# Kernel tuning notes

Measured on AMD Instinct MI355X. Metric: run time of the kernel, lower is better.

The kernel has to match this reference:

```python
import jax, jax.numpy as jnp
import numpy as np

NUM_HEADS = 8
ATTN_DIM = 64

def setup_inputs() -> dict:
    key = jax.random.key(0)
    ks = jax.random.split(key, 16)
    C = ATTN_DIM
    inp = {
        "rgb_fea": jax.random.normal(ks[0], (2, C, 48, 48), jnp.float32),
        "depth_fea": jax.random.normal(ks[1], (2, 1, 24, 24), jnp.float32),
        # expend_conv: Conv2d(1 -> C, k=1), with bias (torch default)
        "w_exp": jax.random.normal(ks[2], (C, 1), jnp.float32) * 0.2,
        "b_exp": jax.random.normal(ks[3], (C,), jnp.float32) * 0.02,
        # q/k/v linears (no bias), weights stored torch-style [out, in]
        "w_rgb_q": jax.random.normal(ks[4], (C, C), jnp.float32) * (C ** -0.5),
        "w_rgb_k": jax.random.normal(ks[5], (C, C), jnp.float32) * (C ** -0.5),
        "w_rgb_v": jax.random.normal(ks[6], (C, C), jnp.float32) * (C ** -0.5),
        "w_dep_q": jax.random.normal(ks[7], (C, C), jnp.float32) * (C ** -0.5),
        "w_dep_k": jax.random.normal(ks[8], (C, C), jnp.float32) * (C ** -0.5),
        "w_dep_v": jax.random.normal(ks[9], (C, C), jnp.float32) * (C ** -0.5),
        # output projections (with bias)
        "w_rgb_proj": jax.random.normal(ks[10], (C, C), jnp.float32) * (C ** -0.5),
        "b_rgb_proj": jax.random.normal(ks[11], (C,), jnp.float32) * 0.02,
        "w_dep_proj": jax.random.normal(ks[12], (C, C), jnp.float32) * (C ** -0.5),
        "b_dep_proj": jax.random.normal(ks[13], (C,), jnp.float32) * 0.02,
        # compress_conv: Conv2d(2C -> C, k=1), with bias
        "w_comp": jax.random.normal(ks[14], (C, 2 * C), jnp.float32) * ((2 * C) ** -0.5),
        "b_comp": jax.random.normal(ks[15], (C,), jnp.float32) * 0.02,
    }
    return inp


def _heads(x, b, n, h):
    # [B, N, C] -> [B, H, N, C/H]
    c = x.shape[-1]
    return x.reshape(b, n, h, c // h).transpose(0, 2, 1, 3)


def reference(rgb_fea, depth_fea, w_exp, b_exp,
              w_rgb_q, w_rgb_k, w_rgb_v, w_dep_q, w_dep_k, w_dep_v,
              w_rgb_proj, b_rgb_proj, w_dep_proj, b_dep_proj,
              w_comp, b_comp):
    b, c, h, w = rgb_fea.shape
    H = NUM_HEADS
    scale = (c // H) ** -0.5

    # expend_conv (1x1) + ReLU + bilinear upsample (align_corners=False)
    d = jnp.einsum('bihw,oi->bohw', depth_fea, w_exp) + b_exp[None, :, None, None]
    d = jax.nn.relu(d)
    d = jax.image.resize(d, (b, c, h, w), method='bilinear')

    # (B,C,H,W) -> transpose(1,3) -> (B,W,H,C) -> (B, N=w*h, C)
    N = w * h
    rgb = rgb_fea.transpose(0, 3, 2, 1).reshape(b, N, c)
    dep = d.transpose(0, 3, 2, 1).reshape(b, N, c)

    rq = _heads(rgb @ w_rgb_q.T, b, N, H)
    rk = _heads(rgb @ w_rgb_k.T, b, N, H)
    rv = _heads(rgb @ w_rgb_v.T, b, N, H)
    dq = _heads(dep @ w_dep_q.T, b, N, H)
    dk = _heads(dep @ w_dep_k.T, b, N, H)
    dv = _heads(dep @ w_dep_v.T, b, N, H)

    # rgb queries attend to depth keys/values
    rgb_attn = jax.nn.softmax(jnp.einsum('bhnd,bhmd->bhnm', rq, dk) * scale, axis=-1)
    rgb_out = jnp.einsum('bhnm,bhmd->bhnd', rgb_attn, dv)
    rgb_out = rgb_out.transpose(0, 2, 1, 3).reshape(b, N, c) @ w_rgb_proj.T + b_rgb_proj

    # depth queries attend to rgb keys/values
    dep_attn = jax.nn.softmax(jnp.einsum('bhnd,bhmd->bhnm', dq, rk) * scale, axis=-1)
    dep_out = jnp.einsum('bhnm,bhmd->bhnd', dep_attn, rv)
    dep_out = dep_out.transpose(0, 2, 1, 3).reshape(b, N, c) @ w_dep_proj.T + b_dep_proj

    # (B,N,C) -> (B,C,N) -> (B,C,w,h)
    rgb_out = rgb_out.transpose(0, 2, 1).reshape(b, c, w, h)
    dep_out = dep_out.transpose(0, 2, 1).reshape(b, c, w, h)

    fuse = jnp.concatenate([rgb_out, dep_out], axis=1)
    fuse = jnp.einsum('bihw,oi->bohw', fuse, w_comp) + b_comp[None, :, None, None]
    return jax.nn.gelu(fuse, approximate=False)
```

## Files before the change

kernel.cpp:

```cpp
#include <hip/hip_runtime.h>
#include <math.h>

#define BATCH 2
#define C 64
#define HH 48
#define WW 48
#define NTOK 2304
#define HEADS 8
#define KVSTRIDE 12

typedef unsigned short bf16_t;
typedef __attribute__((ext_vector_type(8))) short bf16x8;
typedef __attribute__((ext_vector_type(4))) float f32x4;

__device__ __forceinline__ bf16_t f2bf(float f) {
    unsigned int u = __float_as_uint(f);
    u = (u + 0x7fffu + ((u >> 16) & 1u)) >> 16;
    return (bf16_t)u;
}
__device__ __forceinline__ unsigned pack2(float a, float b) {
    return (unsigned)f2bf(a) | ((unsigned)f2bf(b) << 16);
}
__device__ __forceinline__ float4 ld_bf4(const bf16_t* p) {
    uint2 v = *(const uint2*)p;
    float4 r;
    r.x = __uint_as_float(v.x << 16); r.y = __uint_as_float(v.x & 0xffff0000u);
    r.z = __uint_as_float(v.y << 16); r.w = __uint_as_float(v.y & 0xffff0000u);
    return r;
}

__device__ __forceinline__ void stage_x_row(
    float* xrow, const float* rgb, const float* dep,
    const float* w_exp, const float* b_exp,
    int b, int n, int strm, int c0, int cstep)
{
    int wi = n / HH, hi = n % HH;
    if (strm == 0) {
        const float* base = rgb + (size_t)b * C * NTOK + (size_t)hi * WW + wi;
        for (int c = c0; c < 64; c += cstep)
            xrow[c] = base[(size_t)c * NTOK];
    } else {
        float cy = 0.5f * hi - 0.25f, cx = 0.5f * wi - 0.25f;
        float fy0 = floorf(cy), fx0 = floorf(cx);
        float fy = cy - fy0, fx = cx - fx0;
        int y0 = max((int)fy0, 0), x0 = max((int)fx0, 0);
        int y1 = min((int)fy0 + 1, 23), x1 = min((int)fx0 + 1, 23);
        const float* dp = dep + b * 576;
        float d00 = dp[y0*24 + x0], d01 = dp[y0*24 + x1];
        float d10 = dp[y1*24 + x0], d11 = dp[y1*24 + x1];
        for (int c = c0; c < 64; c += cstep) {
            float w = w_exp[c], bb = b_exp[c];
            float r00 = fmaxf(w*d00 + bb, 0.f), r01 = fmaxf(w*d01 + bb, 0.f);
            float r10 = fmaxf(w*d10 + bb, 0.f), r11 = fmaxf(w*d11 + bb, 0.f);
            xrow[c] = (1.f-fy)*((1.f-fx)*r00 + fx*r01) + fy*((1.f-fx)*r10 + fx*r11);
        }
    }
}


__global__ __launch_bounds__(256) void prep_kernel(
    const float* __restrict__ rgb, const float* __restrict__ dep,
    const float* __restrict__ w_exp, const float* __restrict__ b_exp,
    const float* __restrict__ w_rp, const float* __restrict__ w_dp,
    const float* __restrict__ w_comp,
    const float* __restrict__ b_rp, const float* __restrict__ b_dp,
    const float* __restrict__ b_comp,
    float* __restrict__ Xt,
    float* __restrict__ W1, float* __restrict__ W2, float* __restrict__ beff)
{
    __shared__ float U[64*68];
    int bid = blockIdx.x;
    int tid = threadIdx.x;

    if (bid < 144) {
        int t = bid >> 2, z = bid & 3;
        int b = z >> 1, strm = z & 1;
        if (strm == 0) {
            const float* src = rgb + (size_t)b * C * NTOK + t * 64;
            #pragma unroll
            for (int p = 0; p < 4; ++p) {
                int idx = tid + p * 256;
                int c = idx >> 4, m4 = (idx & 15) * 4;
                *(float4*)&U[c*65 + m4] = *(const float4*)&src[(size_t)c * NTOK + m4];
            }
            __syncthreads();
            #pragma unroll
            for (int p = 0; p < 4; ++p) {
                int idx = tid + p * 256;
                int row = idx >> 4, l = idx & 15;
                int mi = t * 64 + row;
                int hi = mi / 48, wi = mi % 48;
                int n  = wi * 48 + hi;
                float4 v;
                v.x = U[(4*l + 0)*65 + row];
                v.y = U[(4*l + 1)*65 + row];
                v.z = U[(4*l + 2)*65 + row];
                v.w = U[(4*l + 3)*65 + row];
                *(float4*)&Xt[((size_t)z * NTOK + n) * 64 + 4*l] = v;
            }
        } else {
            int tok_l = tid >> 2, cq = (tid & 3) * 16;
            int n = t * 64 + tok_l;
            int wi = n / HH, hi = n % HH;
            float cy = 0.5f * hi - 0.25f, cx = 0.5f * wi - 0.25f;
            float fy0 = floorf(cy), fx0 = floorf(cx);
            float fy = cy - fy0, fx = cx - fx0;
            int y0 = max((int)fy0, 0), x0 = max((int)fx0, 0);
            int y1 = min((int)fy0 + 1, 23), x1 = min((int)fx0 + 1, 23);
            const float* dp = dep + b * 576;
            float d00 = dp[y0*24 + x0], d01 = dp[y0*24 + x1];
            float d10 = dp[y1*24 + x0], d11 = dp[y1*24 + x1];
            float* orow = &Xt[((size_t)z * NTOK + n) * 64];
            #pragma unroll
            for (int cc = 0; cc < 16; cc += 4) {
                float4 v;
                #pragma unroll
                for (int j = 0; j < 4; ++j) {
                    int c = cq + cc + j;
                    float w = w_exp[c], bb = b_exp[c];
                    float r00 = fmaxf(w*d00 + bb, 0.f), r01 = fmaxf(w*d01 + bb, 0.f);
                    float r10 = fmaxf(w*d10 + bb, 0.f), r11 = fmaxf(w*d11 + bb, 0.f);
                    ((float*)&v)[j] = (1.f-fy)*((1.f-fx)*r00 + fx*r01)
                                    + fy*((1.f-fx)*r10 + fx*r11);
                }
                *(float4*)&orow[cq + cc] = v;
            }
        }
    } else {
        int idx0 = bid - 144;
        int bx = idx0 & 3, m = idx0 >> 2;
        const float* Wp = m ? w_dp : w_rp;
        float* Wo = m ? W2 : W1;
        int sr = tid >> 4, sc4 = (tid & 15) * 4;
        #pragma unroll
        for (int rr = 0; rr < 4; ++rr) {
            int r = rr*16 + sr;
            *(float4*)&U[r*68 + sc4] = *(const float4*)&Wp[r*64 + sc4];
        }
        __syncthreads();
        int r = tid >> 4;
        int o = bx*16 + r;
        int c4 = (tid & 15) * 4;
        float a0 = 0, a1 = 0, a2 = 0, a3 = 0;
        for (int j = 0; j < 64; ++j) {
            float wc = w_comp[o*128 + m*64 + j];
            float4 wp = *(const float4*)&U[j*68 + c4];
            a0 += wc*wp.x; a1 += wc*wp.y; a2 += wc*wp.z; a3 += wc*wp.w;
        }
        Wo[o*64 + c4]     = a0;
        Wo[o*64 + c4 + 1] = a1;
        Wo[o*64 + c4 + 2] = a2;
        Wo[o*64 + c4 + 3] = a3;
        if (bx == 0 && m == 0 && tid < 64) {
            float s = b_comp[tid];
            for (int j = 0; j < 64; ++j)
                s += w_comp[tid*128 + j] * b_rp[j] + w_comp[tid*128 + 64 + j] * b_dp[j];
            beff[tid] = s;
        }
    }
}

__global__ __launch_bounds__(256) void qkv_kernel(
    const float* __restrict__ Xt,
    const float* __restrict__ w_rq, const float* __restrict__ w_rk,
    const float* __restrict__ w_rv,
    const float* __restrict__ w_dq, const float* __restrict__ w_dk,
    const float* __restrict__ w_dv,
    bf16_t* __restrict__ Qb, bf16_t* __restrict__ Kb, bf16_t* __restrict__ VT)
{
    int tile = blockIdx.x;
    int z    = blockIdx.y;
    int b = z >> 1, strm = z & 1;
    int sb = strm*2 + b;

    __shared__ float Xs[16][68];
    __shared__ float Ws[64][68];
    int tid = threadIdx.x;
    int sr = tid >> 4, sc = (tid & 15) * 4;

    float4 wreg[3][4];
    #pragma unroll
    for (int m = 0; m < 3; ++m) {
        const float* W = strm ? (m == 0 ? w_dq : m == 1 ? w_dk : w_dv)
                              : (m == 0 ? w_rq : m == 1 ? w_rk : w_rv);
        #pragma unroll
        for (int rr = 0; rr < 4; ++rr)
            wreg[m][rr] = *(const float4*)&W[(rr*16 + sr)*64 + sc];
    }
    {
        int row = tid >> 4, c4 = (tid & 15) * 4;
        *(float4*)&Xs[row][c4] =
            *(const float4*)&Xt[((size_t)z*NTOK + tile*16 + row)*64 + c4];
    }

    int ty = tid >> 4, tx = tid & 15;
    #pragma unroll
    for (int m = 0; m < 3; ++m) {
        __syncthreads();
        #pragma unroll
        for (int rr = 0; rr < 4; ++rr)
            *(float4*)&Ws[rr*16 + sr][sc] = wreg[m][rr];
        __syncthreads();

        float acc[4] = {};
        #pragma unroll
        for (int k = 0; k < 64; k += 4) {
            float4 xv = *(const float4*)&Xs[ty][k];
            #pragma unroll
            for (int j = 0; j < 4; ++j) {
                float4 wv = *(const float4*)&Ws[tx + 16*j][k];
                acc[j] += xv.x*wv.x + xv.y*wv.y + xv.z*wv.z + xv.w*wv.w;
            }
        }
        float scale = (m == 0) ? (0.35355339059327373f * 1.4426950408889634f) : 1.0f;
        int n = tile*16 + ty;
        #pragma unroll
        for (int j = 0; j < 4; ++j) {
            int o = tx + 16*j;
            int h = o >> 3, d = o & 7;
            bf16_t v = f2bf(acc[j] * scale);
            if (m == 0)      Qb[(((size_t)sb*8 + h)*NTOK + n)*8 + d] = v;
            else if (m == 1) Kb[(((size_t)sb*8 + h)*NTOK + n)*8 + d] = v;
            else             VT[(((size_t)sb*8 + h)*8 + d)*NTOK + n] = v;
        }
    }
}

__global__ __launch_bounds__(256) void attn_kernel(
    const bf16_t* __restrict__ Qb, const bf16_t* __restrict__ Kb,
    const bf16_t* __restrict__ VT,
    float* __restrict__ AOr, float* __restrict__ AOd)
{
    int h = blockIdx.y;
    int z = blockIdx.z;
    int b = z >> 1, which = z & 1;
    int qsb = which * 2 + b;
    int ksb = (1 - which) * 2 + b;
    const bf16_t* Q  = Qb + ((size_t)qsb * 8 + h) * NTOK * 8;
    const bf16_t* K  = Kb + ((size_t)ksb * 8 + h) * NTOK * 8;
    const bf16_t* Vt = VT + ((size_t)ksb * 8 + h) * 8 * NTOK;
    float* AO = which ? AOd : AOr;

    __shared__ __align__(16) bf16_t Pls[4][2][16][40];
    __shared__ __align__(16) float  Ols[4][16][16];

    int tid = threadIdx.x;
    int t = tid & 63, w = tid >> 6;
    int m16 = t & 15, quad = t >> 4;
    int qt = blockIdx.x * 4 + w;
    int n0 = qt * 16;

    const bf16x8 zf = {0,0,0,0,0,0,0,0};
    const bf16x8 onesf = {0x3F80,0x3F80,0x3F80,0x3F80,
                          0x3F80,0x3F80,0x3F80,0x3F80};
    const f32x4 cz = {0.f, 0.f, 0.f, 0.f};
    bf16_t* PA = &Pls[w][0][0][0];
    bf16_t* PB = &Pls[w][1][0][0];

    bf16x8 qf = (quad == 0) ? *(const bf16x8*)&Q[(size_t)(n0 + m16) * 8] : zf;
    f32x4 oacc = cz;

    auto compute = [&](bf16x8 kA0, bf16x8 kA1, bf16x8 kB0, bf16x8 kB1,
                       bf16x8 vA, bf16x8 vB) {
        f32x4 sA0 = __builtin_amdgcn_mfma_f32_16x16x32_bf16(qf, kA0, cz, 0, 0, 0);
        f32x4 sA1 = __builtin_amdgcn_mfma_f32_16x16x32_bf16(qf, kA1, cz, 0, 0, 0);
        f32x4 sB0 = __builtin_amdgcn_mfma_f32_16x16x32_bf16(qf, kB0, cz, 0, 0, 0);
        f32x4 sB1 = __builtin_amdgcn_mfma_f32_16x16x32_bf16(qf, kB1, cz, 0, 0, 0);
        #pragma unroll
        for (int q4 = 0; q4 < 4; ++q4) {
            float a0 = __builtin_amdgcn_exp2f(sA0[q4]);
            float a1 = __builtin_amdgcn_exp2f(sA1[q4]);
            float b0 = __builtin_amdgcn_exp2f(sB0[q4]);
            float b1 = __builtin_amdgcn_exp2f(sB1[q4]);
            PA[(quad*4 + q4)*40 + m16]      = (bf16_t)(__float_as_uint(a0) >> 16);
            PA[(quad*4 + q4)*40 + m16 + 16] = (bf16_t)(__float_as_uint(a1) >> 16);
            PB[(quad*4 + q4)*40 + m16]      = (bf16_t)(__float_as_uint(b0) >> 16);
            PB[(quad*4 + q4)*40 + m16 + 16] = (bf16_t)(__float_as_uint(b1) >> 16);
        }
        bf16x8 pfA = *(const bf16x8*)&PA[m16*40 + quad * 8];
        oacc = __builtin_amdgcn_mfma_f32_16x16x32_bf16(pfA, vA, oacc, 0, 0, 0);
        bf16x8 pfB = *(const bf16x8*)&PB[m16*40 + quad * 8];
        oacc = __builtin_amdgcn_mfma_f32_16x16x32_bf16(pfB, vB, oacc, 0, 0, 0);
    };

    bf16x8 c0kA0, c0kA1, c0kB0, c0kB1, c0vA, c0vB;
    {
        c0kA0 = (quad == 0) ? *(const bf16x8*)&K[(size_t)(m16) * 8]      : zf;
        c0kA1 = (quad == 0) ? *(const bf16x8*)&K[(size_t)(16 + m16) * 8] : zf;
        c0kB0 = (quad == 0) ? *(const bf16x8*)&K[(size_t)(32 + m16) * 8] : zf;
        c0kB1 = (quad == 0) ? *(const bf16x8*)&K[(size_t)(48 + m16) * 8] : zf;
        c0vA = (m16 < 8) ? *(const bf16x8*)&Vt[(size_t)m16 * NTOK + quad * 8]
             : (m16 == 8 ? onesf : zf);
        c0vB = (m16 < 8) ? *(const bf16x8*)&Vt[(size_t)m16 * NTOK + 32 + quad * 8]
             : (m16 == 8 ? onesf : zf);
    }

    #pragma unroll 1
    for (int cc = 0; cc < 36; cc += 2) {
        int k1 = (cc + 1) * 64;
        bf16x8 c1kA0 = (quad == 0) ? *(const bf16x8*)&K[(size_t)(k1 + m16) * 8]      : zf;
        bf16x8 c1kA1 = (quad == 0) ? *(const bf16x8*)&K[(size_t)(k1 + 16 + m16) * 8] : zf;
        bf16x8 c1kB0 = (quad == 0) ? *(const bf16x8*)&K[(size_t)(k1 + 32 + m16) * 8] : zf;
        bf16x8 c1kB1 = (quad == 0) ? *(const bf16x8*)&K[(size_t)(k1 + 48 + m16) * 8] : zf;
        bf16x8 c1vA = (m16 < 8) ? *(const bf16x8*)&Vt[(size_t)m16 * NTOK + k1 + quad * 8]
                    : (m16 == 8 ? onesf : zf);
        bf16x8 c1vB = (m16 < 8) ? *(const bf16x8*)&Vt[(size_t)m16 * NTOK + k1 + 32 + quad * 8]
                    : (m16 == 8 ? onesf : zf);

        compute(c0kA0, c0kA1, c0kB0, c0kB1, c0vA, c0vB);

        if (cc + 2 < 36) {
            int k2 = (cc + 2) * 64;
            c0kA0 = (quad == 0) ? *(const bf16x8*)&K[(size_t)(k2 + m16) * 8]      : zf;
            c0kA1 = (quad == 0) ? *(const bf16x8*)&K[(size_t)(k2 + 16 + m16) * 8] : zf;
            c0kB0 = (quad == 0) ? *(const bf16x8*)&K[(size_t)(k2 + 32 + m16) * 8] : zf;
            c0kB1 = (quad == 0) ? *(const bf16x8*)&K[(size_t)(k2 + 48 + m16) * 8] : zf;
            c0vA = (m16 < 8) ? *(const bf16x8*)&Vt[(size_t)m16 * NTOK + k2 + quad * 8]
                 : (m16 == 8 ? onesf : zf);
            c0vB = (m16 < 8) ? *(const bf16x8*)&Vt[(size_t)m16 * NTOK + k2 + 32 + quad * 8]
                 : (m16 == 8 ? onesf : zf);
        }

        compute(c1kA0, c1kA1, c1kB0, c1kB1, c1vA, c1vB);
    }

    #pragma unroll
    for (int q4 = 0; q4 < 4; ++q4)
        Ols[w][quad*4 + q4][m16] = oacc[q4];
    #pragma unroll
    for (int e = 0; e < 2; ++e) {
        int idx = t * 2 + e;
        int qq = idx >> 3, d = idx & 7;
        float val = Ols[w][qq][d] / Ols[w][qq][8];
        AO[((size_t)b * NTOK + n0 + qq) * 64 + 8 * h + d] = val;
    }
}

__global__ __launch_bounds__(256) void outcomp_kernel(
    const float* __restrict__ AOr, const float* __restrict__ AOd,
    const float* __restrict__ W1, const float* __restrict__ W2,
    const float* __restrict__ beff, float* __restrict__ out)
{
    int tile = blockIdx.x;
    int b    = blockIdx.y;
    int n0 = tile * 16;
    __shared__ float Ar[16][68];
    __shared__ float Ad[16][68];
    __shared__ float W1s[64][68];
    __shared__ float W2s[64][68];
    int tid = threadIdx.x;
    {
        int row = tid >> 4, c4 = (tid & 15) * 4;
        size_t base = (size_t)b*NTOK + n0 + row;
        *(float4*)&Ar[row][c4] = *(const float4*)&AOr[base*64 + c4];
        *(float4*)&Ad[row][c4] = *(const float4*)&AOd[base*64 + c4];
    }
    {
        int sr = tid >> 4, sc4 = (tid & 15) * 4;
        #pragma unroll
        for (int rr = 0; rr < 4; ++rr) {
            int r = rr*16 + sr;
            *(float4*)&W1s[r][sc4] = *(const float4*)&W1[r*64 + sc4];
            *(float4*)&W2s[r][sc4] = *(const float4*)&W2[r*64 + sc4];
        }
    }
    __syncthreads();

    int tx = tid & 15, ty = tid >> 4;
    float g[4] = {};
    #pragma unroll
    for (int k = 0; k < 64; k += 4) {
        float4 xr = *(const float4*)&Ar[ty][k];
        float4 xd = *(const float4*)&Ad[ty][k];
        #pragma unroll
        for (int jj = 0; jj < 4; ++jj) {
            float4 w1 = *(const float4*)&W1s[tx + 16*jj][k];
            float4 w2 = *(const float4*)&W2s[tx + 16*jj][k];
            g[jj] += xr.x*w1.x + xr.y*w1.y + xr.z*w1.z + xr.w*w1.w
                   + xd.x*w2.x + xd.y*w2.y + xd.z*w2.z + xd.w*w2.w;
        }
    }

    __syncthreads();
    float* Gs = &W1s[0][0];
    #pragma unroll
    for (int jj = 0; jj < 4; ++jj) {
        int o = tx + 16*jj;
        float x = g[jj] + beff[o];
        float gl = 0.5f * x * (1.0f + erff(x * 0.70710678118654752f));
        Gs[o*20 + ty] = gl;
    }
    __syncthreads();
    {
        int o = tid >> 2, s = tid & 3;
        float4 v = *(const float4*)&Gs[o*20 + 4*s];
        *(float4*)&out[((size_t)(b*C + o))*NTOK + n0 + 4*s] = v;
    }
}

__global__ __launch_bounds__(256) void kv_all_kernel(
    const float* __restrict__ rgb, const float* __restrict__ dep,
    const float* __restrict__ w_exp, const float* __restrict__ b_exp,
    const float* __restrict__ w_rk, const float* __restrict__ w_rv,
    const float* __restrict__ w_dk, const float* __restrict__ w_dv,
    bf16_t* __restrict__ Kr, bf16_t* __restrict__ Vr,
    bf16_t* __restrict__ Kd, bf16_t* __restrict__ Vd)
{
    int tile = blockIdx.x;
    int m    = blockIdx.y;
    int z    = blockIdx.z;
    int b = z >> 1, strm = z & 1;
    const float* W = strm ? (m ? w_dv : w_dk) : (m ? w_rv : w_rk);
    bf16_t* O = (strm ? (m ? Vd : Kd) : (m ? Vr : Kr))
              + ((size_t)b * NTOK + tile * 64) * 64;

    __shared__ float Xs[64][68];
    __shared__ float Ws[64][68];
    int tid = threadIdx.x;
    {
        int r = tid & 63, c0 = tid >> 6;
        stage_x_row(&Xs[r][0], rgb, dep, w_exp, b_exp, b, tile*64 + r, strm, c0, 4);
    }
    int sr = tid >> 4, sc = (tid & 15) * 4;
    #pragma unroll
    for (int rr = 0; rr < 4; ++rr) {
        int r = rr*16 + sr;
        *(float4*)&Ws[r][sc] = *(const float4*)&W[r*64 + sc];
    }
    __syncthreads();

    int ty = tid >> 4, tx = tid & 15;
    float acc[4][4] = {};
    #pragma unroll
    for (int k = 0; k < 64; k += 4) {
        float4 xv[4], wv4[4];
        #pragma unroll
        for (int i = 0; i < 4; ++i) xv[i] = *(const float4*)&Xs[4*ty + i][k];
        #pragma unroll
        for (int j = 0; j < 4; ++j) wv4[j] = *(const float4*)&Ws[tx + 16*j][k];
        #pragma unroll
        for (int i = 0; i < 4; ++i)
            #pragma unroll
            for (int j = 0; j < 4; ++j)
                acc[i][j] += xv[i].x*wv4[j].x + xv[i].y*wv4[j].y + xv[i].z*wv4[j].z + xv[i].w*wv4[j].w;
    }
    #pragma unroll
    for (int i = 0; i < 4; ++i)
        #pragma unroll
        for (int j = 0; j < 4; ++j)
            O[(4*ty + i)*64 + tx + 16*j] = f2bf(acc[i][j]);
}

__global__ __launch_bounds__(256) void attn_all_kernel(
    const float* __restrict__ rgb, const float* __restrict__ dep,
    const float* __restrict__ w_exp, const float* __restrict__ b_exp,
    const float* __restrict__ w_rq, const float* __restrict__ w_dq,
    const bf16_t* __restrict__ Kr, const bf16_t* __restrict__ Vr,
    const bf16_t* __restrict__ Kd, const bf16_t* __restrict__ Vd,
    bf16_t* __restrict__ AOr, bf16_t* __restrict__ AOd)
{
    int qt = blockIdx.x;
    int h  = blockIdx.y;
    int z  = blockIdx.z;
    int b = z >> 1, which = z & 1;
    const float* wq = which ? w_dq : w_rq;
    const bf16_t* K = which ? Kr : Kd;
    const bf16_t* V = which ? Vr : Vd;
    bf16_t* AO      = which ? AOd : AOr;

    __shared__ float Xs[64][68];
    __shared__ float Wqs[8][64];
    __shared__ __align__(16) float Ks[4][64][KVSTRIDE];
    __shared__ __align__(16) float Vs[4][64][KVSTRIDE];

    int tid = threadIdx.x;
    int t = tid & 63;
    int w = tid >> 6;
    int n = qt * 64 + t;

    stage_x_row(&Xs[t][0], rgb, dep, w_exp, b_exp, b, n, which == 0 ? 0 : 1, w, 4);
    if (w == 0) {
        #pragma unroll
        for (int d = 0; d < 8; ++d) Wqs[d][t] = wq[(8*h + d)*64 + t];
    }
    __syncthreads();

    const float sc = 0.35355339059327373f * 1.4426950408889634f;
    float q[8];
    #pragma unroll
    for (int d = 0; d < 8; ++d) {
        float s = 0.f;
        #pragma unroll 8
        for (int c = 0; c < 64; ++c) s += Xs[t][c] * Wqs[d][c];
        q[d] = s * sc;
    }

    float mrun = -INFINITY, l = 0.f;
    float acc[8] = {};

    #pragma unroll 1
    for (int st = 0; st < 9; ++st) {
        __syncthreads();
        {
            size_t g = ((size_t)b * NTOK + (w*576 + st*64 + t)) * 64 + 8 * h;
            *(float4*)&Ks[w][t][0] = ld_bf4(&K[g]);
            *(float4*)&Ks[w][t][4] = ld_bf4(&K[g + 4]);
            *(float4*)&Vs[w][t][0] = ld_bf4(&V[g]);
            *(float4*)&Vs[w][t][4] = ld_bf4(&V[g + 4]);
        }
        __syncthreads();

        for (int g8 = 0; g8 < 8; ++g8) {
            float s[8];
            #pragma unroll
            for (int u = 0; u < 8; ++u) {
                const float4 ka = *(const float4*)&Ks[w][g8*8 + u][0];
                const float4 kb = *(const float4*)&Ks[w][g8*8 + u][4];
                s[u] = q[0]*ka.x + q[1]*ka.y + q[2]*ka.z + q[3]*ka.w
                     + q[4]*kb.x + q[5]*kb.y + q[6]*kb.z + q[7]*kb.w;
            }
            float tm = fmaxf(fmaxf(fmaxf(s[0],s[1]), fmaxf(s[2],s[3])),
                             fmaxf(fmaxf(s[4],s[5]), fmaxf(s[6],s[7])));
            float mn = fmaxf(mrun, tm);
            float alpha = __builtin_amdgcn_exp2f(mrun - mn);
            float ps = 0.f;
            #pragma unroll
            for (int u = 0; u < 8; ++u) { s[u] = __builtin_amdgcn_exp2f(s[u] - mn); ps += s[u]; }
            l = l * alpha + ps;
            #pragma unroll
            for (int d = 0; d < 8; ++d) acc[d] *= alpha;
            #pragma unroll
            for (int u = 0; u < 8; ++u) {
                const float4 va = *(const float4*)&Vs[w][g8*8 + u][0];
                const float4 vb = *(const float4*)&Vs[w][g8*8 + u][4];
                acc[0] += s[u]*va.x; acc[1] += s[u]*va.y; acc[2] += s[u]*va.z; acc[3] += s[u]*va.w;
                acc[4] += s[u]*vb.x; acc[5] += s[u]*vb.y; acc[6] += s[u]*vb.z; acc[7] += s[u]*vb.w;
            }
            mrun = mn;
        }
    }

    float* part = &Xs[0][0];
    __syncthreads();
    {
        float* p = &part[(w*64 + t) * 10];
        p[0] = mrun; p[1] = l;
        #pragma unroll
        for (int d = 0; d < 8; ++d) p[2 + d] = acc[d];
    }
    __syncthreads();
    if (tid < 64) {
        float M = -INFINITY;
        #pragma unroll
        for (int v = 0; v < 4; ++v) M = fmaxf(M, part[(v*64 + t)*10]);
        float L = 0.f, o[8] = {};
        #pragma unroll
        for (int v = 0; v < 4; ++v) {
            const float* p = &part[(v*64 + t)*10];
            float al = __builtin_amdgcn_exp2f(p[0] - M);
            L += p[1] * al;
            #pragma unroll
            for (int d = 0; d < 8; ++d) o[d] += p[2 + d] * al;
        }
        float inv = 1.0f / L;
        uint4 ov;
        ov.x = pack2(o[0]*inv, o[1]*inv);
        ov.y = pack2(o[2]*inv, o[3]*inv);
        ov.z = pack2(o[4]*inv, o[5]*inv);
        ov.w = pack2(o[6]*inv, o[7]*inv);
        *(uint4*)&AO[((size_t)b * NTOK + n) * 64 + 8 * h] = ov;
    }
}

__global__ __launch_bounds__(256) void projcomp_all_kernel(
    const bf16_t* __restrict__ AOr, const bf16_t* __restrict__ AOd,
    const float* __restrict__ w_rp, const float* __restrict__ b_rp,
    const float* __restrict__ w_dp, const float* __restrict__ b_dp,
    const float* __restrict__ w_comp, const float* __restrict__ b_comp,
    float* __restrict__ out)
{
    int tile = blockIdx.x;
    int b    = blockIdx.y;
    __shared__ float A[64][68];
    __shared__ float Bf[64][68];
    __shared__ float Pf[64][68];
    int tid = threadIdx.x;
    int sr = tid >> 4, sc = (tid & 15) * 4;
    int ty = tid >> 4, tx = tid & 15;
    float G[4][4] = {};

    #pragma unroll
    for (int half = 0; half < 2; ++half) {
        const bf16_t* AOx = half ? AOd : AOr;
        const float* Wp   = half ? w_dp : w_rp;
        const float* bp   = half ? b_dp : b_rp;
        #pragma unroll
        for (int rr = 0; rr < 4; ++rr) {
            int r = rr*16 + sr;
            *(float4*)&A[r][sc]  = ld_bf4(&AOx[((size_t)b*NTOK + tile*64 + r)*64 + sc]);
            *(float4*)&Bf[r][sc] = *(const float4*)&Wp[r*64 + sc];
        }
        __syncthreads();
        float acc[4][4] = {};
        #pragma unroll
        for (int k = 0; k < 64; k += 4) {
            float4 xv[4], wv[4];
            #pragma unroll
            for (int i = 0; i < 4; ++i) xv[i] = *(const float4*)&A[4*ty + i][k];
            #pragma unroll
            for (int j = 0; j < 4; ++j) wv[j] = *(const float4*)&Bf[tx + 16*j][k];
            #pragma unroll
            for (int i = 0; i < 4; ++i)
                #pragma unroll
                for (int j = 0; j < 4; ++j)
                    acc[i][j] += xv[i].x*wv[j].x + xv[i].y*wv[j].y + xv[i].z*wv[j].z + xv[i].w*wv[j].w;
        }
        __syncthreads();
        #pragma unroll
        for (int j = 0; j < 4; ++j) {
            float bj = bp[tx + 16*j];
            #pragma unroll
            for (int i = 0; i < 4; ++i)
                Pf[4*ty + i][tx + 16*j] = acc[i][j] + bj;
        }
        #pragma unroll
        for (int rr = 0; rr < 4; ++rr) {
            int r = rr*16 + sr;
            *(float4*)&Bf[r][sc] = *(const float4*)&w_comp[r*128 + half*64 + sc];
        }
        __syncthreads();
        #pragma unroll
        for (int k = 0; k < 64; k += 4) {
            float4 xv[4], wv[4];
            #pragma unroll
            for (int i = 0; i < 4; ++i) xv[i] = *(const float4*)&Pf[4*ty + i][k];
            #pragma unroll
            for (int j = 0; j < 4; ++j) wv[j] = *(const float4*)&Bf[tx + 16*j][k];
            #pragma unroll
            for (int i = 0; i < 4; ++i)
                #pragma unroll
                for (int j = 0; j < 4; ++j)
                    G[i][j] += xv[i].x*wv[j].x + xv[i].y*wv[j].y + xv[i].z*wv[j].z + xv[i].w*wv[j].w;
        }
        __syncthreads();
    }

    #pragma unroll
    for (int j = 0; j < 4; ++j) {
        int o = tx + 16*j;
        float bj = b_comp[o];
        #pragma unroll
        for (int i = 0; i < 4; ++i) {
            int n = tile*64 + 4*ty + i;
            int wi = n / HH, hi = n % HH;
            float x = G[i][j] + bj;
            float g = 0.5f * x * (1.0f + erff(x * 0.70710678118654752f));
            out[((b*C + o)*WW + wi)*HH + hi] = g;
        }
    }
}

extern "C" void kernel_launch(void* const* d_in, const int* in_sizes, int n_in,
                              void* d_out, int out_size, void* d_ws, size_t ws_size,
                              hipStream_t stream) {
    const float* rgb_fea = (const float*)d_in[0];
    const float* depth   = (const float*)d_in[1];
    const float* w_exp   = (const float*)d_in[2];
    const float* b_exp   = (const float*)d_in[3];
    const float* w_rq    = (const float*)d_in[4];
    const float* w_rk    = (const float*)d_in[5];
    const float* w_rv    = (const float*)d_in[6];
    const float* w_dq    = (const float*)d_in[7];
    const float* w_dk    = (const float*)d_in[8];
    const float* w_dv    = (const float*)d_in[9];
    const float* w_rp    = (const float*)d_in[10];
    const float* b_rp    = (const float*)d_in[11];
    const float* w_dp    = (const float*)d_in[12];
    const float* b_dp    = (const float*)d_in[13];
    const float* w_comp  = (const float*)d_in[14];
    const float* b_comp  = (const float*)d_in[15];
    float* out = (float*)d_out;

    if (ws_size >= 5931264) {
        char* Wb = (char*)d_ws;
        bf16_t* Qb   = (bf16_t*)Wb;
        bf16_t* Kb   = (bf16_t*)(Wb + 1179648);
        bf16_t* VT   = (bf16_t*)(Wb + 2359296);
        float*  XtAO = (float*)(Wb + 3538944);
        float*  AOr  = XtAO;
        float*  AOd  = XtAO + 294912;
        float*  W1   = (float*)(Wb + 5898240);
        float*  W2   = (float*)(Wb + 5914624);
        float*  beff = (float*)(Wb + 5931008);
        float*  Xt   = XtAO;

        prep_kernel<<<dim3(152), dim3(256), 0, stream>>>(
            rgb_fea, depth, w_exp, b_exp, w_rp, w_dp, w_comp,
            b_rp, b_dp, b_comp, Xt, W1, W2, beff);
        qkv_kernel<<<dim3(144, 4), dim3(256), 0, stream>>>(
            Xt, w_rq, w_rk, w_rv, w_dq, w_dk, w_dv, Qb, Kb, VT);
        attn_kernel<<<dim3(36, 8, 4), dim3(256), 0, stream>>>(
            Qb, Kb, VT, AOr, AOd);
        outcomp_kernel<<<dim3(144, 2), dim3(256), 0, stream>>>(
            AOr, AOd, W1, W2, beff, out);
    } else {
        const size_t BUF = (size_t)BATCH * NTOK * 64;
        bf16_t* Kr  = (bf16_t*)d_ws;
        bf16_t* Vr  = Kr + BUF;
        bf16_t* Kd  = Vr + BUF;
        bf16_t* Vd  = Kd + BUF;
        bf16_t* AOr = Vd + BUF;
        bf16_t* AOd = AOr + BUF;
        kv_all_kernel<<<dim3(36, 2, 4), dim3(256), 0, stream>>>(
            rgb_fea, depth, w_exp, b_exp, w_rk, w_rv, w_dk, w_dv, Kr, Vr, Kd, Vd);
        attn_all_kernel<<<dim3(36, 8, 4), dim3(256), 0, stream>>>(
            rgb_fea, depth, w_exp, b_exp, w_rq, w_dq, Kr, Vr, Kd, Vd, AOr, AOd);
        projcomp_all_kernel<<<dim3(36, 2), dim3(256), 0, stream>>>(
            AOr, AOd, w_rp, b_rp, w_dp, b_dp, w_comp, b_comp, out);
    }
}
```

Measured before the change: 170.0 us.

## Transpose score MFMA to write P with vector LDS stores, drop double buffering

The attention loop now computes scores as K·Q (swapped MFMA operands), so each lane owns a row of P and can write four bf16 values with one vector LDS store instead of scalar stores. The chunk size drops from 64 to 32 keys per iteration, and the manual two-stage register prefetch of K/V is removed in favour of a simple loop. This cuts LDS store instructions and register pressure, but loses the explicit load/compute overlap and adds more loop iterations.

Result: faster. 166.4 us (-2.1%).

```diff
diff --git a/kernel.cpp b/kernel.cpp
--- a/kernel.cpp
+++ b/kernel.cpp
@@ -11,6 +11,7 @@
 
 typedef unsigned short bf16_t;
 typedef __attribute__((ext_vector_type(8))) short bf16x8;
+typedef __attribute__((ext_vector_type(4))) short bf16x4;
 typedef __attribute__((ext_vector_type(4))) float f32x4;
 
 __device__ __forceinline__ bf16_t f2bf(float f) {
@@ -241,7 +242,7 @@
     const bf16_t* Vt = VT + ((size_t)ksb * 8 + h) * 8 * NTOK;
     float* AO = which ? AOd : AOr;
 
-    __shared__ __align__(16) bf16_t Pls[4][2][16][40];
+    __shared__ __align__(16) bf16_t Pls[4][16][40];
     __shared__ __align__(16) float  Ols[4][16][16];
 
     int tid = threadIdx.x;
@@ -254,79 +255,40 @@
     const bf16x8 onesf = {0x3F80,0x3F80,0x3F80,0x3F80,
                           0x3F80,0x3F80,0x3F80,0x3F80};
     const f32x4 cz = {0.f, 0.f, 0.f, 0.f};
-    bf16_t* PA = &Pls[w][0][0][0];
-    bf16_t* PB = &Pls[w][1][0][0];
 
     bf16x8 qf = (quad == 0) ? *(const bf16x8*)&Q[(size_t)(n0 + m16) * 8] : zf;
+
     f32x4 oacc = cz;
 
-    auto compute = [&](bf16x8 kA0, bf16x8 kA1, bf16x8 kB0, bf16x8 kB1,
-                       bf16x8 vA, bf16x8 vB) {
-        f32x4 sA0 = __builtin_amdgcn_mfma_f32_16x16x32_bf16(qf, kA0, cz, 0, 0, 0);
-        f32x4 sA1 = __builtin_amdgcn_mfma_f32_16x16x32_bf16(qf, kA1, cz, 0, 0, 0);
-        f32x4 sB0 = __builtin_amdgcn_mfma_f32_16x16x32_bf16(qf, kB0, cz, 0, 0, 0);
-        f32x4 sB1 = __builtin_amdgcn_mfma_f32_16x16x32_bf16(qf, kB1, cz, 0, 0, 0);
-        #pragma unroll
-        for (int q4 = 0; q4 < 4; ++q4) {
-            float a0 = __builtin_amdgcn_exp2f(sA0[q4]);
-            float a1 = __builtin_amdgcn_exp2f(sA1[q4]);
-            float b0 = __builtin_amdgcn_exp2f(sB0[q4]);
-            float b1 = __builtin_amdgcn_exp2f(sB1[q4]);
-            PA[(quad*4 + q4)*40 + m16]      = (bf16_t)(__float_as_uint(a0) >> 16);
-            PA[(quad*4 + q4)*40 + m16 + 16] = (bf16_t)(__float_as_uint(a1) >> 16);
-            PB[(quad*4 + q4)*40 + m16]      = (bf16_t)(__float_as_uint(b0) >> 16);
-            PB[(quad*4 + q4)*40 + m16 + 16] = (bf16_t)(__float_as_uint(b1) >> 16);
-        }
-        bf16x8 pfA = *(const bf16x8*)&PA[m16*40 + quad * 8];
-        oacc = __builtin_amdgcn_mfma_f32_16x16x32_bf16(pfA, vA, oacc, 0, 0, 0);
-        bf16x8 pfB = *(const bf16x8*)&PB[m16*40 + quad * 8];
-        oacc = __builtin_amdgcn_mfma_f32_16x16x32_bf16(pfB, vB, oacc, 0, 0, 0);
-    };
-
-    bf16x8 c0kA0, c0kA1, c0kB0, c0kB1, c0vA, c0vB;
-    {
-        c0kA0 = (quad == 0) ? *(const bf16x8*)&K[(size_t)(m16) * 8]      : zf;
-        c0kA1 = (quad == 0) ? *(const bf16x8*)&K[(size_t)(16 + m16) * 8] : zf;
-        c0kB0 = (quad == 0) ? *(const bf16x8*)&K[(size_t)(32 + m16) * 8] : zf;
-        c0kB1 = (quad == 0) ? *(const bf16x8*)&K[(size_t)(48 + m16) * 8] : zf;
-        c0vA = (m16 < 8) ? *(const bf16x8*)&Vt[(size_t)m16 * NTOK + quad * 8]
-             : (m16 == 8 ? onesf : zf);
-        c0vB = (m16 < 8) ? *(const bf16x8*)&Vt[(size_t)m16 * NTOK + 32 + quad * 8]
-             : (m16 == 8 ? onesf : zf);
-    }
-
     #pragma unroll 1
-    for (int cc = 0; cc < 36; cc += 2) {
-        int k1 = (cc + 1) * 64;
-        bf16x8 c1kA0 = (quad == 0) ? *(const bf16x8*)&K[(size_t)(k1 + m16) * 8]      : zf;
-        bf16x8 c1kA1 = (quad == 0) ? *(const bf16x8*)&K[(size_t)(k1 + 16 + m16) * 8] : zf;
-        bf16x8 c1kB0 = (quad == 0) ? *(const bf16x8*)&K[(size_t)(k1 + 32 + m16) * 8] : zf;
-        bf16x8 c1kB1 = (quad == 0) ? *(const bf16x8*)&K[(size_t)(k1 + 48 + m16) * 8] : zf;
-        bf16x8 c1vA = (m16 < 8) ? *(const bf16x8*)&Vt[(size_t)m16 * NTOK + k1 + quad * 8]
-                    : (m16 == 8 ? onesf : zf);
-        bf16x8 c1vB = (m16 < 8) ? *(const bf16x8*)&Vt[(size_t)m16 * NTOK + k1 + 32 + quad * 8]
-                    : (m16 == 8 ? onesf : zf);
-
-        compute(c0kA0, c0kA1, c0kB0, c0kB1, c0vA, c0vB);
-
-        if (cc + 2 < 36) {
-            int k2 = (cc + 2) * 64;
-            c0kA0 = (quad == 0) ? *(const bf16x8*)&K[(size_t)(k2 + m16) * 8]      : zf;
-            c0kA1 = (quad == 0) ? *(const bf16x8*)&K[(size_t)(k2 + 16 + m16) * 8] : zf;
-            c0kB0 = (quad == 0) ? *(const bf16x8*)&K[(size_t)(k2 + 32 + m16) * 8] : zf;
-            c0kB1 = (quad == 0) ? *(const bf16x8*)&K[(size_t)(k2 + 48 + m16) * 8] : zf;
-            c0vA = (m16 < 8) ? *(const bf16x8*)&Vt[(size_t)m16 * NTOK + k2 + quad * 8]
-                 : (m16 == 8 ? onesf : zf);
-            c0vB = (m16 < 8) ? *(const bf16x8*)&Vt[(size_t)m16 * NTOK + k2 + 32 + quad * 8]
-                 : (m16 == 8 ? onesf : zf);
-        }
-
-        compute(c1kA0, c1kA1, c1kB0, c1kB1, c1vA, c1vB);
-    }
-
-    #pragma unroll
-    for (int q4 = 0; q4 < 4; ++q4)
-        Ols[w][quad*4 + q4][m16] = oacc[q4];
+    for (int ck = 0; ck < 72; ++ck) {
+        int k0 = ck * 32;
+        bf16x8 kf0 = (quad == 0) ? *(const bf16x8*)&K[(size_t)(k0 + m16) * 8]      : zf;
+        bf16x8 kf1 = (quad == 0) ? *(const bf16x8*)&K[(size_t)(k0 + 16 + m16) * 8] : zf;
+        bf16x8 vf = (m16 < 8) ? *(const bf16x8*)&Vt[(size_t)m16 * NTOK + k0 + quad * 8]
+                  : (m16 == 8 ? onesf : zf);
+
+        f32x4 s0 = __builtin_amdgcn_mfma_f32_16x16x32_bf16(kf0, qf, cz, 0, 0, 0);
+        f32x4 s1 = __builtin_amdgcn_mfma_f32_16x16x32_bf16(kf1, qf, cz, 0, 0, 0);
+
+        bf16x4 pA, pB;
+        #pragma unroll
+        for (int r = 0; r < 4; ++r) {
+            float p0 = __builtin_amdgcn_exp2f(s0[r]);
+            float p1 = __builtin_amdgcn_exp2f(s1[r]);
+            pA[r] = (short)(__float_as_uint(p0) >> 16);
+            pB[r] = (short)(__float_as_uint(p1) >> 16);
+        }
+        *(bf16x4*)&Pls[w][m16][quad * 4]      = pA;
+        *(bf16x4*)&Pls[w][m16][16 + quad * 4] = pB;
+
+        bf16x8 pf = *(const bf16x8*)&Pls[w][m16][quad * 8];
+        oacc = __builtin_amdgcn_mfma_f32_16x16x32_bf16(pf, vf, oacc, 0, 0, 0);
+    }
+
+    #pragma unroll
+    for (int r = 0; r < 4; ++r)
+        Ols[w][quad*4 + r][m16] = oacc[r];
     #pragma unroll
     for (int e = 0; e < 2; ++e) {
         int idx = t * 2 + e;
```
